# Optimization experiments

Hardware: AMD Instinct MI355X
Metric: run time of the kernel (lower is better)

## Reference

```python
import jax, jax.numpy as jnp
import numpy as np

# static config (matches init_kwargs and spatial_shapes input)
SPATIAL = ((100, 100), (50, 50), (25, 25), (13, 13))  # (H, W) per level
D_MODEL, N_HEADS, N_LEVELS, N_POINTS, D_FFN = 256, 8, 4, 4, 1024
D_HEAD = D_MODEL // N_HEADS
LEN_IN = sum(h * w for h, w in SPATIAL)
LEVEL_START = np.cumsum([0] + [h * w for h, w in SPATIAL])[:-1]


def setup_inputs() -> dict:
    key = jax.random.key(0)
    ks = jax.random.split(key, 12)
    N = 2
    f = lambda k, shape, s=0.02: jax.random.normal(k, shape, jnp.float32) * s
    return {
        "src": jax.random.normal(ks[0], (N, LEN_IN, D_MODEL), jnp.float32),
        "pos": jax.random.normal(ks[1], (N, LEN_IN, D_MODEL), jnp.float32),
        "reference_points": jax.random.uniform(ks[2], (N, LEN_IN, N_LEVELS, 2), jnp.float32),
        "spatial_shapes": jnp.asarray(SPATIAL, jnp.int32),
        "level_start_index": jnp.asarray(LEVEL_START, jnp.int32),
        "W_value": f(ks[3], (D_MODEL, D_MODEL)),
        "b_value": jnp.zeros((D_MODEL,), jnp.float32),
        "W_off": f(ks[4], (D_MODEL, N_HEADS * N_LEVELS * N_POINTS * 2)),
        "b_off": f(ks[5], (N_HEADS * N_LEVELS * N_POINTS * 2,), 0.5),
        "W_attn": f(ks[6], (D_MODEL, N_HEADS * N_LEVELS * N_POINTS)),
        "b_attn": jnp.zeros((N_HEADS * N_LEVELS * N_POINTS,), jnp.float32),
        "W_out": f(ks[7], (D_MODEL, D_MODEL)),
        "b_out": jnp.zeros((D_MODEL,), jnp.float32),
        "W1": f(ks[8], (D_MODEL, D_FFN)),
        "b1": jnp.zeros((D_FFN,), jnp.float32),
        "W2": f(ks[9], (D_FFN, D_MODEL)),
        "b2": jnp.zeros((D_MODEL,), jnp.float32),
        "g1": jnp.ones((D_MODEL,), jnp.float32),
        "be1": jnp.zeros((D_MODEL,), jnp.float32),
        "g2": jnp.ones((D_MODEL,), jnp.float32),
        "be2": jnp.zeros((D_MODEL,), jnp.float32),
    }


def _ln(x, g, b, eps=1e-5):
    mu = x.mean(-1, keepdims=True)
    var = ((x - mu) ** 2).mean(-1, keepdims=True)
    return (x - mu) * jax.lax.rsqrt(var + eps) * g + b


def _bilinear(v, loc, H, W):
    # v: [N, heads, H*W, Dh]; loc: [N, Lq, heads, P, 2] normalized to [0,1]
    # replicates F.grid_sample(align_corners=False, padding_mode='zeros') with grid=2*loc-1
    N, Lq, Hh, P, _ = loc.shape
    x = loc[..., 0] * W - 0.5
    y = loc[..., 1] * H - 0.5
    x0 = jnp.floor(x)
    y0 = jnp.floor(y)
    wx1 = x - x0
    wy1 = y - y0
    x0i = x0.astype(jnp.int32)
    y0i = y0.astype(jnp.int32)
    out = jnp.zeros((N, Lq, Hh, P, v.shape[-1]), v.dtype)
    for dy, dx in ((0, 0), (0, 1), (1, 0), (1, 1)):
        xi = x0i + dx
        yi = y0i + dy
        w = (wx1 if dx else 1.0 - wx1) * (wy1 if dy else 1.0 - wy1)
        valid = (xi >= 0) & (xi < W) & (yi >= 0) & (yi < H)
        idx = jnp.clip(yi, 0, H - 1) * W + jnp.clip(xi, 0, W - 1)  # [N,Lq,Hh,P]
        idx = idx.transpose(0, 2, 1, 3).reshape(N, Hh, Lq * P)
        g = jax.vmap(jax.vmap(lambda vm, im: vm[im]))(v, idx)  # [N,Hh,Lq*P,Dh]
        g = g.reshape(N, Hh, Lq, P, -1).transpose(0, 2, 1, 3, 4)
        out = out + (w * valid)[..., None] * g
    return out


def reference(src, pos, reference_points, spatial_shapes, level_start_index,
              W_value, b_value, W_off, b_off, W_attn, b_attn, W_out, b_out,
              W1, b1, W2, b2, g1, be1, g2, be2):
    N, Lq, _ = src.shape
    value = (src @ W_value + b_value).reshape(N, Lq, N_HEADS, D_HEAD)
    q = src + pos  # with_pos_embed
    off = (q @ W_off + b_off).reshape(N, Lq, N_HEADS, N_LEVELS, N_POINTS, 2)
    attn = (q @ W_attn + b_attn).reshape(N, Lq, N_HEADS, N_LEVELS * N_POINTS)
    attn = jax.nn.softmax(attn, axis=-1).reshape(N, Lq, N_HEADS, N_LEVELS, N_POINTS)
    # offset_normalizer = (W, H) per level
    normalizer = jnp.asarray([[w, h] for h, w in SPATIAL], jnp.float32)
    loc = reference_points[:, :, None, :, None, :] + off / normalizer[None, None, None, :, None, :]
    out = jnp.zeros((N, Lq, N_HEADS, D_HEAD), jnp.float32)
    for l, (H, W) in enumerate(SPATIAL):
        s = int(LEVEL_START[l])
        v_l = value[:, s:s + H * W].transpose(0, 2, 1, 3)  # [N, heads, H*W, Dh]
        samp = _bilinear(v_l, loc[:, :, :, l], H, W)       # [N, Lq, heads, P, Dh]
        out = out + jnp.einsum('nqhp,nqhpc->nqhc', attn[:, :, :, l], samp)
    src2 = out.reshape(N, Lq, D_MODEL) @ W_out + b_out
    x = _ln(src + src2, g1, be1)
    ffn = jax.nn.relu(x @ W1 + b1) @ W2 + b2
    return _ln(x + ffn, g2, be2)
```

## Files before the change

kernel.cpp:

```cpp
#include <hip/hip_runtime.h>
#include <hip/hip_bf16.h>
#include <cstdint>

#define D_MODEL   256
#define N_HEADS   8
#define N_LEVELS  4
#define N_POINTS  4
#define D_FFN     1024
#define D_HEAD    32
#define LEN_IN    13294
#define NBATCH    2
#define M_TOK     (NBATCH * LEN_IN)
#define M_PAD     26624

__constant__ int c_lvl_h[4] = {100, 50, 25, 13};
__constant__ int c_lvl_w[4] = {100, 50, 25, 13};
__constant__ int c_lvl_s[4] = {0, 10000, 12500, 13125};

typedef __attribute__((ext_vector_type(8))) __bf16 bf16x8;
typedef __attribute__((ext_vector_type(4))) __bf16 bf16x4;
typedef __attribute__((ext_vector_type(4))) float  f32x4;
typedef __attribute__((ext_vector_type(4))) uint32_t u32x4;

__device__ __forceinline__ float bflo(uint32_t w) { return __uint_as_float(w << 16); }
__device__ __forceinline__ float bfhi(uint32_t w) { return __uint_as_float(w & 0xffff0000u); }

__device__ __forceinline__ void lds_direct16(const void* g, void* l) {
    __builtin_amdgcn_global_load_lds(
        (const __attribute__((address_space(1))) uint32_t*)(uintptr_t)g,
        (__attribute__((address_space(3))) uint32_t*)(uintptr_t)l,
        16, 0, 0);
}

__global__ __launch_bounds__(256) void prep(
    const float* __restrict__ s0, const float* __restrict__ s1, const float* __restrict__ s2,
    const float* __restrict__ s3, const float* __restrict__ s4, const float* __restrict__ s5,
    __bf16* __restrict__ d0, __bf16* __restrict__ d1, __bf16* __restrict__ d2,
    __bf16* __restrict__ d3, __bf16* __restrict__ d4, __bf16* __restrict__ d5,
    const float* __restrict__ b_off, const float* __restrict__ b_attn,
    float* __restrict__ bias_oa,
    const float4* __restrict__ src, const float4* __restrict__ pos,
    bf16x4* __restrict__ sb, bf16x4* __restrict__ qb, int n4)
{
    const int tid = threadIdx.x;
    const int b = blockIdx.x;
    if (b >= 737) {
        const int i = (b - 737) * 256 + tid;
        if (i >= n4) return;
        const float4 s = src[i];
        const float4 p = pos[i];
        bf16x4 sv = { (__bf16)s.x, (__bf16)s.y, (__bf16)s.z, (__bf16)s.w };
        bf16x4 qv = { (__bf16)(s.x + p.x), (__bf16)(s.y + p.y),
                      (__bf16)(s.z + p.z), (__bf16)(s.w + p.w) };
        sb[i] = sv;
        qb[i] = qv;
        return;
    }
    if (b == 736) {
        if (tid < 256) bias_oa[tid] = b_off[tid];
        if (tid < 128) bias_oa[256 + tid] = b_attn[tid];
        return;
    }
    const int tx = tid & 31;
    const int ty = tid >> 5;
    const int starts[7] = {0, 64, 128, 160, 224, 480, 736};
    const int Ks[6] = {256, 256, 256, 256, 256, 1024};
    const int Ns[6] = {256, 256, 128, 256, 1024, 256};
    const float* srcs[6] = {s0, s1, s2, s3, s4, s5};
    __bf16* dsts[6] = {d0, d1, d2, d3, d4, d5};
    int i = 0;
    while (b >= starts[i + 1]) ++i;
    const int t = b - starts[i];
    const int K = Ks[i], N = Ns[i];
    const float* W = srcs[i];
    __bf16* Wt = dsts[i];
    const int ntx = N >> 5;
    const int n0 = (t % ntx) * 32;
    const int k0 = (t / ntx) * 32;

    __shared__ float tl[32][33];
    #pragma unroll
    for (int j = 0; j < 4; ++j)
        tl[ty + j * 8][tx] = W[(size_t)(k0 + ty + j * 8) * N + n0 + tx];
    __syncthreads();
    #pragma unroll
    for (int j = 0; j < 4; ++j)
        Wt[(size_t)(n0 + ty + j * 8) * K + k0 + tx] = (__bf16)tl[tx][ty + j * 8];
}

template <bool RELU, int K, bool HEADMAJOR>
__device__ __forceinline__ void gemm_core(
    const __bf16* __restrict__ A, const __bf16* __restrict__ Bt,
    const float* __restrict__ bias, __bf16* __restrict__ C,
    int M, int N, int bm, int bn)
{
    __shared__ __bf16 smem[17408];
    __bf16* As = smem;
    __bf16* Bs = smem + 8192;

    const int tid  = threadIdx.x;
    const int lane = tid & 63;
    const int wv   = tid >> 6;
    const int wm   = (wv >> 1) * 64;
    const int wn   = (wv & 1) * 64;
    const int srow = lane >> 2;
    const int skc  = (lane & 3) * 8;
    const int fm   = lane & 15;
    const int fko  = (lane >> 4) * 8;

    f32x4 acc[4][4] = {};

    for (int k0 = 0; k0 < K; k0 += 64) {
        #pragma unroll
        for (int p = 0; p < 2; ++p) {
            #pragma unroll
            for (int c = 0; c < 2; ++c) {
                const int r = wv * 32 + c * 16;
                lds_direct16(A  + (size_t)(bm + r + srow) * K + k0 + p * 32 + skc, As + p * 4096 + r * 32);
                lds_direct16(Bt + (size_t)(bn + r + srow) * K + k0 + p * 32 + skc, Bs + p * 4096 + r * 32);
            }
        }
        __syncthreads();

        #pragma unroll
        for (int p = 0; p < 2; ++p) {
            bf16x8 af[4], bfr[4];
            #pragma unroll
            for (int t = 0; t < 4; ++t) {
                af[t]  = *(const bf16x8*)(As + p * 4096 + (wm + t * 16 + fm) * 32 + fko);
                bfr[t] = *(const bf16x8*)(Bs + p * 4096 + (wn + t * 16 + fm) * 32 + fko);
            }
            #pragma unroll
            for (int mt = 0; mt < 4; ++mt)
                #pragma unroll
                for (int nt = 0; nt < 4; ++nt)
                    acc[mt][nt] = __builtin_amdgcn_mfma_f32_16x16x32_bf16(
                        af[mt], bfr[nt], acc[mt][nt], 0, 0, 0);
        }
        __syncthreads();
    }

    const int ecol = lane & 15;
    const int erow = (lane >> 4) * 4;
    #pragma unroll
    for (int nt = 0; nt < 4; ++nt) {
        const int cl = wn + nt * 16 + ecol;
        const float bv = bias[bn + cl];
        #pragma unroll
        for (int mt = 0; mt < 4; ++mt) {
            #pragma unroll
            for (int r = 0; r < 4; ++r) {
                const int rl = wm + mt * 16 + erow + r;
                float v = acc[mt][nt][r] + bv;
                if (RELU) v = fmaxf(v, 0.f);
                smem[rl * 136 + cl] = (__bf16)v;
            }
        }
    }
    __syncthreads();
    #pragma unroll
    for (int rr = 0; rr < 8; ++rr) {
        const int idx = rr * 256 + tid;
        const int row = idx >> 4;
        const int ch  = idx & 15;
        if (bm + row < M) {
            if (HEADMAJOR) {
                const int col = bn + ch * 8;
                *(bf16x8*)(C + ((size_t)(col >> 5) * M_PAD + (bm + row)) * 32 + (col & 31)) =
                    *(const bf16x8*)(smem + row * 136 + ch * 8);
            } else {
                *(bf16x8*)(C + (size_t)(bm + row) * N + bn + ch * 8) =
                    *(const bf16x8*)(smem + row * 136 + ch * 8);
            }
        }
    }
}

__global__ __launch_bounds__(256) void gemm_front(
    const __bf16* __restrict__ A0, const __bf16* __restrict__ B0,
    const float* __restrict__ bi0, __bf16* __restrict__ C0,
    const __bf16* __restrict__ A1, const __bf16* __restrict__ B1,
    const float* __restrict__ bi1, __bf16* __restrict__ C1, int M)
{
    const int bx = blockIdx.x;
    if (bx < 2)
        gemm_core<false, 256, true>(A0, B0, bi0, C0, M, 256, blockIdx.y * 128, bx * 128);
    else
        gemm_core<false, 256, false>(A1, B1, bi1, C1, M, 384, blockIdx.y * 128, (bx - 2) * 128);
}

__global__ __launch_bounds__(256) void gemm_ffn1(
    const __bf16* __restrict__ A, const __bf16* __restrict__ Bt,
    const float* __restrict__ bias, __bf16* __restrict__ C, int M)
{
    gemm_core<true, 256, false>(A, Bt, bias, C, M, 1024, blockIdx.y * 128, blockIdx.x * 128);
}

template <typename OutT, int K>
__global__ __launch_bounds__(256) void gemm_ln32(
    const __bf16* __restrict__ A, const __bf16* __restrict__ Bt,
    const float* __restrict__ bias, const __bf16* __restrict__ res,
    const float* __restrict__ gamma, const float* __restrict__ beta,
    OutT* __restrict__ Cout, int M)
{
    __shared__ __bf16 smem[18432];
    __bf16* As = smem;
    __bf16* Bs = smem + 2048;
    __shared__ float lnsum[32][4];
    __shared__ float lnsq[32][4];
    __shared__ float lnstat[32][2];

    const int tid  = threadIdx.x;
    const int lane = tid & 63;
    const int wv   = tid >> 6;
    const int bm   = blockIdx.x * 32;
    const int wn   = wv * 64;
    const int srow = lane >> 2;
    const int skc  = (lane & 3) * 8;
    const int fm   = lane & 15;
    const int fko  = (lane >> 4) * 8;

    f32x4 acc[2][4] = {};

    for (int k0 = 0; k0 < K; k0 += 64) {
        {
            const int p  = wv >> 1;
            const int rh = (wv & 1) * 16;
            lds_direct16(A + (size_t)(bm + rh + srow) * K + k0 + p * 32 + skc,
                         As + p * 1024 + rh * 32);
        }
        #pragma unroll
        for (int p = 0; p < 2; ++p) {
            #pragma unroll
            for (int c = 0; c < 4; ++c) {
                const int r = wv * 64 + c * 16;
                lds_direct16(Bt + (size_t)(r + srow) * K + k0 + p * 32 + skc,
                             Bs + p * 8192 + r * 32);
            }
        }
        __syncthreads();

        #pragma unroll
        for (int p = 0; p < 2; ++p) {
            bf16x8 af[2], bfr[4];
            #pragma unroll
            for (int mt = 0; mt < 2; ++mt)
                af[mt] = *(const bf16x8*)(As + p * 1024 + (mt * 16 + fm) * 32 + fko);
            #pragma unroll
            for (int nt = 0; nt < 4; ++nt)
                bfr[nt] = *(const bf16x8*)(Bs + p * 8192 + (wn + nt * 16 + fm) * 32 + fko);
            #pragma unroll
            for (int mt = 0; mt < 2; ++mt)
                #pragma unroll
                for (int nt = 0; nt < 4; ++nt)
                    acc[mt][nt] = __builtin_amdgcn_mfma_f32_16x16x32_bf16(
                        af[mt], bfr[nt], acc[mt][nt], 0, 0, 0);
        }
        __syncthreads();
    }

    const int ecol = lane & 15;
    const int erow = (lane >> 4) * 4;

    float g4[4], b4[4];
    #pragma unroll
    for (int nt = 0; nt < 4; ++nt) {
        const int col = wn + nt * 16 + ecol;
        g4[nt] = gamma[col];
        b4[nt] = beta[col];
        const float bv = bias[col];
        #pragma unroll
        for (int mt = 0; mt < 2; ++mt) {
            #pragma unroll
            for (int r = 0; r < 4; ++r) {
                const int row = bm + mt * 16 + erow + r;
                acc[mt][nt][r] += bv + (float)res[(size_t)row * 256 + col];
            }
        }
    }

    #pragma unroll
    for (int mt = 0; mt < 2; ++mt) {
        #pragma unroll
        for (int r = 0; r < 4; ++r) {
            float s  = acc[mt][0][r] + acc[mt][1][r] + acc[mt][2][r] + acc[mt][3][r];
            float s2 = acc[mt][0][r] * acc[mt][0][r] + acc[mt][1][r] * acc[mt][1][r]
                     + acc[mt][2][r] * acc[mt][2][r] + acc[mt][3][r] * acc[mt][3][r];
            #pragma unroll
            for (int o = 1; o < 16; o <<= 1) {
                s  += __shfl_xor(s, o);
                s2 += __shfl_xor(s2, o);
            }
            if (ecol == 0) {
                const int rl = mt * 16 + erow + r;
                lnsum[rl][wv] = s;
                lnsq[rl][wv]  = s2;
            }
        }
    }
    __syncthreads();
    if (tid < 32) {
        const float s  = lnsum[tid][0] + lnsum[tid][1] + lnsum[tid][2] + lnsum[tid][3];
        const float s2 = lnsq[tid][0] + lnsq[tid][1] + lnsq[tid][2] + lnsq[tid][3];
        const float mu = s * (1.f / 256.f);
        const float var = s2 * (1.f / 256.f) - mu * mu;
        lnstat[tid][0] = mu;
        lnstat[tid][1] = rsqrtf(var + 1e-5f);
    }
    __syncthreads();

    if constexpr (sizeof(OutT) == 2) {
        __bf16* ct = smem;
        #pragma unroll
        for (int mt = 0; mt < 2; ++mt) {
            #pragma unroll
            for (int r = 0; r < 4; ++r) {
                const int rl = mt * 16 + erow + r;
                const float mu = lnstat[rl][0];
                const float rs = lnstat[rl][1];
                #pragma unroll
                for (int nt = 0; nt < 4; ++nt) {
                    const int col = wn + nt * 16 + ecol;
                    ct[rl * 264 + col] = (__bf16)((acc[mt][nt][r] - mu) * rs * g4[nt] + b4[nt]);
                }
            }
        }
        __syncthreads();
        #pragma unroll
        for (int rr = 0; rr < 4; ++rr) {
            const int idx = rr * 256 + tid;
            const int row = idx >> 5;
            const int ch  = idx & 31;
            if (bm + row < M)
                *(bf16x8*)((__bf16*)Cout + (size_t)(bm + row) * 256 + ch * 8) =
                    *(const bf16x8*)(ct + row * 264 + ch * 8);
        }
    } else {
        float* ct = (float*)smem;
        #pragma unroll
        for (int mt = 0; mt < 2; ++mt) {
            #pragma unroll
            for (int r = 0; r < 4; ++r) {
                const int rl = mt * 16 + erow + r;
                const float mu = lnstat[rl][0];
                const float rs = lnstat[rl][1];
                #pragma unroll
                for (int nt = 0; nt < 4; ++nt) {
                    const int col = wn + nt * 16 + ecol;
                    ct[rl * 260 + col] = (acc[mt][nt][r] - mu) * rs * g4[nt] + b4[nt];
                }
            }
        }
        __syncthreads();
        #pragma unroll
        for (int rr = 0; rr < 8; ++rr) {
            const int idx = rr * 256 + tid;
            const int row = idx >> 6;
            const int ch  = idx & 63;
            if (bm + row < M) {
                float4 v = *(const float4*)(ct + row * 260 + ch * 4);
                *(float4*)((float*)Cout + (size_t)(bm + row) * 256 + ch * 4) = v;
            }
        }
    }
}

__global__ __launch_bounds__(256) void msda_sample(
    const __bf16* __restrict__ value,
    const __bf16* __restrict__ oa,
    const float* __restrict__ refp,
    __bf16* __restrict__ out)
{
    __shared__ uint32_t sc[32 * 132];
    __shared__ float sw[32][16];

    const int tid = threadIdx.x;
    const int blk = blockIdx.x;

    if (tid < 32) {
        const int t = tid >> 3;
        const int h = tid & 7;
        const int row = blk * 4 + t;
        const __bf16* ap = oa + (size_t)row * 384 + 256 + h * 16;
        const bf16x8 v0 = *(const bf16x8*)ap;
        const bf16x8 v1 = *(const bf16x8*)(ap + 8);
        float e[16];
        #pragma unroll
        for (int i = 0; i < 8; ++i) { e[i] = (float)v0[i]; e[8 + i] = (float)v1[i]; }
        float mx = -1e30f;
        #pragma unroll
        for (int i = 0; i < 16; ++i) mx = fmaxf(mx, e[i]);
        float s = 0.f;
        #pragma unroll
        for (int i = 0; i < 16; ++i) { e[i] = __expf(e[i] - mx); s += e[i]; }
        const float inv = 1.f / s;
        #pragma unroll
        for (int i = 0; i < 16; ++i) sw[tid][i] = e[i] * inv;
    }
    __syncthreads();

    #pragma unroll
    for (int it = 0; it < 2; ++it) {
        const int idx = it * 256 + tid;
        const int t  = idx >> 7;
        const int h  = (idx >> 4) & 7;
        const int lp = idx & 15;
        const int l  = lp >> 2;
        const int row = blk * 4 + t;
        const int Ww = c_lvl_w[l];
        const int Hh = c_lvl_h[l];
        const uint32_t opk = *(const uint32_t*)(oa + (size_t)row * 384 + h * 32 + lp * 2);
        const float ox = bflo(opk), oy = bfhi(opk);
        const float rx = refp[((size_t)row * 4 + l) * 2 + 0];
        const float ry = refp[((size_t)row * 4 + l) * 2 + 1];
        const float x = (rx + ox / (float)Ww) * (float)Ww - 0.5f;
        const float y = (ry + oy / (float)Hh) * (float)Hh - 0.5f;
        const float xf = floorf(x), yf = floorf(y);
        const float fx = x - xf,    fy = y - yf;
        const int x0 = (int)xf, y0 = (int)yf;
        const int n  = (row >= LEN_IN) ? 1 : 0;
        const int lvlbase = n * LEN_IN + c_lvl_s[l];
        const float a = sw[t * 8 + h][lp];
        const int xs = min(max(x0, 0), Ww - 2);
        const int d  = x0 - xs;
        const float wxl = 1.f - fx, wxr = fx;
        const float pw0 = (d == 0) ? wxl : ((d == -1) ? wxr : 0.f);
        const float pw1 = (d == 0) ? wxr : ((d == 1) ? wxl : 0.f);
        uint32_t* p = sc + (t * 8 + h) * 132 + lp * 8;
        #pragma unroll
        for (int dy = 0; dy < 2; ++dy) {
            const int yi = y0 + dy;
            const int yc = min(max(yi, 0), Hh - 1);
            const bool yv = (yi >= 0) & (yi < Hh);
            const float wy = (dy ? fy : 1.f - fy) * (yv ? a : 0.f);
            const uint32_t boff = (uint32_t)(lvlbase + yc * Ww + xs) * 64u;
            u32x4 pk = { boff, __float_as_uint(pw0 * wy), __float_as_uint(pw1 * wy), 0u };
            *(u32x4*)(p + dy * 4) = pk;
        }
    }
    __syncthreads();

    const int t  = tid >> 6;
    const int h  = (tid >> 3) & 7;
    const int c8 = tid & 7;
    const uint32_t* mb = sc + (t * 8 + h) * 132;
    const char* __restrict__ vpb = (const char*)(value + (size_t)h * (M_PAD * 32));
    const uint32_t lsub = (uint32_t)c8 * 16u;
    const bool hi = (c8 >= 4);
    float acc[8] = {};
    #pragma unroll 8
    for (int qd = 0; qd < 32; ++qd) {
        const u32x4 md = *(const u32x4*)(mb + qd * 4);
        const float w = __uint_as_float(hi ? md.z : md.y);
        const u32x4 v = *(const u32x4*)(vpb + (size_t)(md.x + lsub));
        #pragma unroll
        for (int d2 = 0; d2 < 4; ++d2) {
            acc[2 * d2]     += w * bflo(v[d2]);
            acc[2 * d2 + 1] += w * bfhi(v[d2]);
        }
    }
    #pragma unroll
    for (int j = 0; j < 8; ++j) acc[j] += __shfl_xor(acc[j], 4);
    if (c8 < 4) {
        bf16x8 o;
        #pragma unroll
        for (int j = 0; j < 8; ++j) o[j] = (__bf16)acc[j];
        const int orow = blk * 4 + t;
        *(bf16x8*)(out + (size_t)orow * 256 + h * 32 + c8 * 8) = o;
    }
}

extern "C" void kernel_launch(void* const* d_in, const int* in_sizes, int n_in,
                              void* d_out, int out_size, void* d_ws, size_t ws_size,
                              hipStream_t stream)
{
    const float* src     = (const float*)d_in[0];
    const float* pos     = (const float*)d_in[1];
    const float* refp    = (const float*)d_in[2];
    const float* W_value = (const float*)d_in[5];
    const float* b_value = (const float*)d_in[6];
    const float* W_off   = (const float*)d_in[7];
    const float* b_off   = (const float*)d_in[8];
    const float* W_attn  = (const float*)d_in[9];
    const float* b_attn  = (const float*)d_in[10];
    const float* W_out   = (const float*)d_in[11];
    const float* b_out   = (const float*)d_in[12];
    const float* W1      = (const float*)d_in[13];
    const float* b1      = (const float*)d_in[14];
    const float* W2      = (const float*)d_in[15];
    const float* b2      = (const float*)d_in[16];
    const float* g1      = (const float*)d_in[17];
    const float* be1     = (const float*)d_in[18];
    const float* g2      = (const float*)d_in[19];
    const float* be2     = (const float*)d_in[20];
    float* outp = (float*)d_out;

    const int M = M_TOK;
    char* ws = (char*)d_ws;
    const size_t R2 = (size_t)M_PAD * 512;

    __bf16* src_b = (__bf16*)(ws);
    __bf16* q_b   = (__bf16*)(ws + R2);
    __bf16* val_b = (__bf16*)(ws + 2 * R2);
    __bf16* oa    = (__bf16*)(ws + 3 * R2);
    __bf16* samp  = (__bf16*)(ws + 9 * R2 / 2);
    __bf16* x_b   = (__bf16*)(ws + 11 * R2 / 2);
    __bf16* hbuf  = (__bf16*)(ws);
    __bf16* wbase = (__bf16*)(ws + 13 * R2 / 2);
    __bf16* Wt_value = wbase;
    __bf16* Wt_oa    = wbase + 65536;
    __bf16* Wt_out   = wbase + 163840;
    __bf16* Wt1      = wbase + 229376;
    __bf16* Wt2      = wbase + 491520;
    float*  bias_oa  = (float*)(wbase + 753664);

    const dim3 blk(256);
    const int n4 = M * 256 / 4;
    const int gm = M_PAD / 128;

    prep<<<dim3(737 + (n4 + 255) / 256), blk, 0, stream>>>(
        W_value, W_off, W_attn, W_out, W1, W2,
        Wt_value, Wt_oa, Wt_oa + 65536, Wt_out, Wt1, Wt2,
        b_off, b_attn, bias_oa,
        (const float4*)src, (const float4*)pos, (bf16x4*)src_b, (bf16x4*)q_b, n4);

    gemm_front<<<dim3(5, gm), blk, 0, stream>>>(
        src_b, Wt_value, b_value, val_b,
        q_b,   Wt_oa,    bias_oa, oa, M);

    msda_sample<<<dim3(M / 4), blk, 0, stream>>>(val_b, oa, refp, samp);

    gemm_ln32<__bf16, 256><<<dim3(M_PAD / 32), blk, 0, stream>>>(
        samp, Wt_out, b_out, src_b, g1, be1, x_b, M);

    gemm_ffn1<<<dim3(8, gm), blk, 0, stream>>>(x_b, Wt1, b1, hbuf, M);

    gemm_ln32<float, 1024><<<dim3(M_PAD / 32), blk, 0, stream>>>(
        hbuf, Wt2, b2, x_b, g2, be2, outp, M);
}
```

Baseline: 299.2 us.

## Halve LDS in fused GEMM+LayerNorm kernels and coalesce head-major stores

The GEMM+LayerNorm kernel now stages a K-step of 32 instead of 64, which halves its shared-memory tile. The fp32 output epilogue is split into two 16-row halves so the staging buffer fits the smaller allocation, and launch bounds request 5 blocks per CU. The aim is higher occupancy to hide latency, paid for with twice as many K-loop iterations and barriers. The head-major store in the front GEMM is also reordered so each 32-column head plane is written with contiguous 64-byte rows.

```diff
diff --git a/kernel.cpp b/kernel.cpp
--- a/kernel.cpp
+++ b/kernel.cpp
@@ -161,17 +161,19 @@
     #pragma unroll
     for (int rr = 0; rr < 8; ++rr) {
         const int idx = rr * 256 + tid;
-        const int row = idx >> 4;
-        const int ch  = idx & 15;
-        if (bm + row < M) {
-            if (HEADMAJOR) {
-                const int col = bn + ch * 8;
-                *(bf16x8*)(C + ((size_t)(col >> 5) * M_PAD + (bm + row)) * 32 + (col & 31)) =
-                    *(const bf16x8*)(smem + row * 136 + ch * 8);
-            } else {
+        if (HEADMAJOR) {
+            const int plane = idx >> 9;
+            const int row   = (idx >> 2) & 127;
+            const int ch4   = idx & 3;
+            if (bm + row < M)
+                *(bf16x8*)(C + ((size_t)((bn >> 5) + plane) * M_PAD + (bm + row)) * 32 + ch4 * 8) =
+                    *(const bf16x8*)(smem + row * 136 + plane * 32 + ch4 * 8);
+        } else {
+            const int row = idx >> 4;
+            const int ch  = idx & 15;
+            if (bm + row < M)
                 *(bf16x8*)(C + (size_t)(bm + row) * N + bn + ch * 8) =
                     *(const bf16x8*)(smem + row * 136 + ch * 8);
-            }
         }
     }
 }
@@ -197,15 +199,15 @@
 }
 
 template <typename OutT, int K>
-__global__ __launch_bounds__(256) void gemm_ln32(
+__global__ __launch_bounds__(256, 5) void gemm_ln(
     const __bf16* __restrict__ A, const __bf16* __restrict__ Bt,
     const float* __restrict__ bias, const __bf16* __restrict__ res,
     const float* __restrict__ gamma, const float* __restrict__ beta,
     OutT* __restrict__ Cout, int M)
 {
-    __shared__ __bf16 smem[18432];
+    __shared__ __bf16 smem[9216];
     __bf16* As = smem;
-    __bf16* Bs = smem + 2048;
+    __bf16* Bs = smem + 1024;
     __shared__ float lnsum[32][4];
     __shared__ float lnsq[32][4];
     __shared__ float lnstat[32][2];
@@ -222,40 +224,30 @@
 
     f32x4 acc[2][4] = {};
 
-    for (int k0 = 0; k0 < K; k0 += 64) {
-        {
-            const int p  = wv >> 1;
-            const int rh = (wv & 1) * 16;
-            lds_direct16(A + (size_t)(bm + rh + srow) * K + k0 + p * 32 + skc,
-                         As + p * 1024 + rh * 32);
-        }
-        #pragma unroll
-        for (int p = 0; p < 2; ++p) {
-            #pragma unroll
-            for (int c = 0; c < 4; ++c) {
-                const int r = wv * 64 + c * 16;
-                lds_direct16(Bt + (size_t)(r + srow) * K + k0 + p * 32 + skc,
-                             Bs + p * 8192 + r * 32);
-            }
+    for (int k0 = 0; k0 < K; k0 += 32) {
+        if (tid < 128)
+            lds_direct16(A + (size_t)(bm + (tid >> 2)) * K + k0 + (tid & 3) * 8,
+                         As + tid * 8);
+        #pragma unroll
+        for (int c = 0; c < 4; ++c) {
+            const int r = wv * 64 + c * 16;
+            lds_direct16(Bt + (size_t)(r + srow) * K + k0 + skc, Bs + r * 32);
         }
         __syncthreads();
 
-        #pragma unroll
-        for (int p = 0; p < 2; ++p) {
-            bf16x8 af[2], bfr[4];
-            #pragma unroll
-            for (int mt = 0; mt < 2; ++mt)
-                af[mt] = *(const bf16x8*)(As + p * 1024 + (mt * 16 + fm) * 32 + fko);
+        bf16x8 af[2], bfr[4];
+        #pragma unroll
+        for (int mt = 0; mt < 2; ++mt)
+            af[mt] = *(const bf16x8*)(As + (mt * 16 + fm) * 32 + fko);
+        #pragma unroll
+        for (int nt = 0; nt < 4; ++nt)
+            bfr[nt] = *(const bf16x8*)(Bs + (wn + nt * 16 + fm) * 32 + fko);
+        #pragma unroll
+        for (int mt = 0; mt < 2; ++mt)
             #pragma unroll
             for (int nt = 0; nt < 4; ++nt)
-                bfr[nt] = *(const bf16x8*)(Bs + p * 8192 + (wn + nt * 16 + fm) * 32 + fko);
-            #pragma unroll
-            for (int mt = 0; mt < 2; ++mt)
-                #pragma unroll
-                for (int nt = 0; nt < 4; ++nt)
-                    acc[mt][nt] = __builtin_amdgcn_mfma_f32_16x16x32_bf16(
-                        af[mt], bfr[nt], acc[mt][nt], 0, 0, 0);
-        }
+                acc[mt][nt] = __builtin_amdgcn_mfma_f32_16x16x32_bf16(
+                    af[mt], bfr[nt], acc[mt][nt], 0, 0, 0);
         __syncthreads();
     }
 
@@ -338,29 +330,33 @@
     } else {
         float* ct = (float*)smem;
         #pragma unroll
-        for (int mt = 0; mt < 2; ++mt) {
+        for (int hf = 0; hf < 2; ++hf) {
+            const int mt = hf;
             #pragma unroll
             for (int r = 0; r < 4; ++r) {
-                const int rl = mt * 16 + erow + r;
+                const int rl   = mt * 16 + erow + r;
+                const int rloc = erow + r;
                 const float mu = lnstat[rl][0];
                 const float rs = lnstat[rl][1];
                 #pragma unroll
                 for (int nt = 0; nt < 4; ++nt) {
                     const int col = wn + nt * 16 + ecol;
-                    ct[rl * 260 + col] = (acc[mt][nt][r] - mu) * rs * g4[nt] + b4[nt];
+                    ct[rloc * 260 + col] = (acc[mt][nt][r] - mu) * rs * g4[nt] + b4[nt];
                 }
             }
-        }
-        __syncthreads();
-        #pragma unroll
-        for (int rr = 0; rr < 8; ++rr) {
-            const int idx = rr * 256 + tid;
-            const int row = idx >> 6;
-            const int ch  = idx & 63;
-            if (bm + row < M) {
-                float4 v = *(const float4*)(ct + row * 260 + ch * 4);
-                *(float4*)((float*)Cout + (size_t)(bm + row) * 256 + ch * 4) = v;
-            }
+            __syncthreads();
+            #pragma unroll
+            for (int rr = 0; rr < 4; ++rr) {
+                const int idx = rr * 256 + tid;
+                const int row = idx >> 6;
+                const int ch  = idx & 63;
+                const int grow = bm + hf * 16 + row;
+                if (grow < M) {
+                    float4 v = *(const float4*)(ct + row * 260 + ch * 4);
+                    *(float4*)((float*)Cout + (size_t)grow * 256 + ch * 4) = v;
+                }
+            }
+            __syncthreads();
         }
     }
 }
@@ -530,11 +526,11 @@
 
     msda_sample<<<dim3(M / 4), blk, 0, stream>>>(val_b, oa, refp, samp);
 
-    gemm_ln32<__bf16, 256><<<dim3(M_PAD / 32), blk, 0, stream>>>(
+    gemm_ln<__bf16, 256><<<dim3(M_PAD / 32), blk, 0, stream>>>(
         samp, Wt_out, b_out, src_b, g1, be1, x_b, M);
 
     gemm_ffn1<<<dim3(8, gm), blk, 0, stream>>>(x_b, Wt1, b1, hbuf, M);
 
-    gemm_ln32<float, 1024><<<dim3(M_PAD / 32), blk, 0, stream>>>(
+    gemm_ln<float, 1024><<<dim3(M_PAD / 32), blk, 0, stream>>>(
         hbuf, Wt2, b2, x_b, g2, be2, outp, M);
 }
```

After: 301.7 us. No clear change (+0.8%).
